# Optimization experiments

Hardware: AMD Instinct MI355X
Metric: run time of the kernel (lower is better)

Reference implementation:

```python
import jax, jax.numpy as jnp
import numpy as np

B, N, D = 1, 128, 64
H, DH = 8, 64            # heads, per-head dim; dim_inner = dim*dim_head = 512
DI = H * DH              # 512
L = 2                    # max_degree
S = 1 + 2 * L            # 5 degree slots: (h, r_1..L, x_1..L)
MLP = 1024               # int(2.0 * dim_inner)
EPS = 1e-5


def _ln(x, g):
    m = x.mean(-1, keepdims=True)
    v = ((x - m) ** 2).mean(-1, keepdims=True)
    return (x - m) * jax.lax.rsqrt(v + EPS) * g


def setup_inputs() -> dict:
    key = jax.random.key(0)
    ks = jax.random.split(key, 16)
    rn = lambda k, s, sc=1.0: jax.random.normal(k, s, dtype=jnp.float32) * sc
    return {
        "h": rn(ks[0], (B, N, D)),
        "t_ij": rn(ks[1], (B, N, N, D)),
        "r1": rn(ks[2], (B, N, N, 3)),
        "r2": rn(ks[3], (B, N, N, 5)),
        "x1": rn(ks[4], (B, N, D, 3)),
        "x2": rn(ks[5], (B, N, D, 5)),
        "g_hi": jnp.ones((D,), jnp.float32),
        "g_hj": jnp.ones((D,), jnp.float32),
        "Wq": rn(ks[6], (D, DI), D ** -0.5),
        "Wk": rn(ks[7], (D, DI), D ** -0.5),
        "Wv1": rn(ks[8], (D, MLP), D ** -0.5),
        "bv1": jnp.zeros((MLP,), jnp.float32),
        "Wv2": rn(ks[9], (MLP, S * DI), MLP ** -0.5),
        "bv2": jnp.zeros((S * DI,), jnp.float32),
        "Wp1": rn(ks[10], (D, MLP), D ** -0.5),
        "bp1": jnp.zeros((MLP,), jnp.float32),
        "Wp2": rn(ks[11], (MLP, S * DI), MLP ** -0.5),
        "bp2": jnp.zeros((S * DI,), jnp.float32),
        "Wev": rn(ks[12], (D, S * DI), D ** -0.5),
        "Wc": rn(ks[13], (DI, D), DI ** -0.5),
    }


def reference(h, t_ij, r1, r2, x1, x2, g_hi, g_hj, Wq, Wk, Wv1, bv1, Wv2, bv2,
              Wp1, bp1, Wp2, bp2, Wev, Wc):
    b, n, d = h.shape
    hi, hj = _ln(h, g_hi), _ln(h, g_hj)
    q = (hi @ Wq).reshape(b, n, H, DH).transpose(0, 2, 1, 3)                # b h i d
    k = (hj @ Wk).reshape(b, n, H, DH).transpose(0, 2, 1, 3)                # b h j d
    vals = (jax.nn.silu(hj @ Wv1 + bv1) @ Wv2 + bv2)
    vals = vals.reshape(b, n, S, H, DH).transpose(0, 3, 1, 2, 4)            # b h j s d
    pav = (jax.nn.silu(hj @ Wp1 + bp1) @ Wp2 + bp2)
    pav = pav.reshape(b, n, S, H, DH).transpose(0, 3, 1, 2, 4)              # b h j s d
    # NOTE: source uses to_edge_values for BOTH edge keys and edge values (to_edge_keys is dead code)
    ev = (t_ij @ Wev).reshape(b, n, n, S, H, DH).transpose(0, 4, 1, 2, 3, 5)  # b h i j s d
    sim_num = jnp.einsum('bhid,bhjd->bhij', q, k)                           # b h i j
    sim_den = jnp.einsum('bhid,bhijsd->bhis', q, ev)                        # b h i s
    attn = sim_num[..., None] / sim_den[:, :, :, None, :]                   # b h i j s (quotient attention)
    sea = attn[..., None] * vals[:, :, None] + ev * pav[:, :, None]         # b h i j s d
    out = sea.transpose(0, 2, 3, 4, 1, 5).reshape(b, n, n, S, DI) @ Wc      # b i j s D
    # split sizes (1, L, L) along the s axis: h scale, r_ij scales, x scales
    h_new = h + out[:, :, :, 0, :].sum(axis=2)                              # sum over neighbors j
    xs, rs = (x1, x2), (r1, r2)
    x_new = [jnp.einsum('bjdm,bijd->bidm', xs[l], out[:, :, :, 1 + L + l, :])
             + jnp.einsum('bijm,bijd->bidm', rs[l], out[:, :, :, 1 + l, :])
             for l in range(L)]
    return (h_new, x_new[0], x_new[1])
```

## Files before the change

kernel.cpp:

```cpp
#include <hip/hip_runtime.h>
#include <hip/hip_bf16.h>

typedef __hip_bfloat16 bf16;
typedef __attribute__((ext_vector_type(8))) short short8;
typedef __attribute__((ext_vector_type(4))) float f32x4;

#define NN 128
#define DD_ 64
#define HH_ 8
#define DH_ 64
#define DI_ 512
#define SS_ 5
#define MLPD 1024
#define SDI 2560

__device__ __forceinline__ float wave_sum64(float v) {
#pragma unroll
    for (int off = 32; off > 0; off >>= 1) v += __shfl_xor(v, off, 64);
    return v;
}

__device__ __forceinline__ unsigned short f2bf_u(float f) {
    unsigned u = __float_as_uint(f);
    u += 0x7FFF + ((u >> 16) & 1);
    return (unsigned short)(u >> 16);
}
__device__ __forceinline__ float bfu2f(unsigned short s) {
    return __uint_as_float(((unsigned)s) << 16);
}
__device__ __forceinline__ unsigned pk2(unsigned short a, unsigned short b) {
    return (unsigned)a | ((unsigned)b << 16);
}

__global__ __launch_bounds__(256) void k_front(
    const float* __restrict__ h, const float* __restrict__ ghi, const float* __restrict__ ghj,
    const float* __restrict__ Wq, const float* __restrict__ Wk,
    const float* __restrict__ Wv1, const float* __restrict__ bv1,
    const float* __restrict__ Wp1, const float* __restrict__ bp1,
    float* __restrict__ q, float* __restrict__ k,
    float* __restrict__ a1, float* __restrict__ p1) {
    int i = blockIdx.x, ch = blockIdx.y, t = threadIdx.x;
    int d = t & 63;
    __shared__ float hib[DD_], hjb[DD_];
    float x = h[i * DD_ + d];
    float s = wave_sum64(x);
    float s2 = wave_sum64(x * x);
    float m = s * (1.0f / DD_);
    float v = s2 * (1.0f / DD_) - m * m;
    float r = rsqrtf(v + 1e-5f);
    float xc = (x - m) * r;
    if (t < 64) { hib[d] = xc * ghi[d]; hjb[d] = xc * ghj[d]; }
    __syncthreads();
    {
        int c = ch * 128 + (t & 127);
        const float* W = (t < 128) ? Wq : Wk;
        const float* hb = (t < 128) ? hib : hjb;
        float a = 0.f;
#pragma unroll 8
        for (int dd = 0; dd < DD_; dd++) a += hb[dd] * W[dd * DI_ + c];
        float* dstqk = (t < 128) ? q : k;
        dstqk[i * DI_ + c] = a;
    }
    {
        int c = ch * 256 + t;
        float av = 0.f, ap = 0.f;
#pragma unroll 4
        for (int dd = 0; dd < DD_; dd++) {
            float hv = hjb[dd];
            av += hv * Wv1[dd * MLPD + c];
            ap += hv * Wp1[dd * MLPD + c];
        }
        float xv = av + bv1[c], xp = ap + bp1[c];
        a1[i * MLPD + c] = xv / (1.0f + expf(-xv));
        p1[i * MLPD + c] = xp / (1.0f + expf(-xp));
    }
}

#define KS2 4
__global__ __launch_bounds__(256) void k_mlp2(const float* __restrict__ a1,
                                              const float* __restrict__ p1,
                                              const float* __restrict__ Wv2,
                                              const float* __restrict__ Wp2,
                                              float* __restrict__ part) {
    int ct = blockIdx.x, ks = blockIdx.y, t = threadIdx.x;
    int c0 = ct * 64;
    bool isp = c0 >= 2560;
    int c0l = c0 - (isp ? 2560 : 0);
    const float* __restrict__ src = isp ? p1 : a1;
    const float* __restrict__ W = isp ? Wp2 : Wv2;
    int kbase = ks * 256;
    __shared__ unsigned short Ahi[128][40], Alo[128][40];
    __shared__ unsigned short Bhi[64][40], Blo[64][40];
    int lane = t & 63, wv = t >> 6;
    int l15 = lane & 15, quad = lane >> 4;
    f32x4 acc[2][4];
#pragma unroll
    for (int mt = 0; mt < 2; mt++)
#pragma unroll
        for (int nt = 0; nt < 4; nt++) acc[mt][nt] = (f32x4){0.f, 0.f, 0.f, 0.f};
    int aj = t >> 1, ak = (t & 1) * 16;
    int bc = t & 63, bk = (t >> 6) * 8;
    for (int kc = 0; kc < 8; kc++) {
        int k0 = kbase + kc * 32;
        __syncthreads();
        {
            unsigned short h16[16], l16[16];
            const float* ap = &src[(size_t)aj * MLPD + k0 + ak];
#pragma unroll
            for (int e = 0; e < 16; e += 4) {
                float4 v = *(const float4*)(ap + e);
                float vv[4] = {v.x, v.y, v.z, v.w};
#pragma unroll
                for (int z = 0; z < 4; z++) {
                    unsigned short hb = f2bf_u(vv[z]);
                    h16[e + z] = hb;
                    l16[e + z] = f2bf_u(vv[z] - bfu2f(hb));
                }
            }
            *(uint4*)&Ahi[aj][ak] = make_uint4(pk2(h16[0], h16[1]), pk2(h16[2], h16[3]),
                                               pk2(h16[4], h16[5]), pk2(h16[6], h16[7]));
            *(uint4*)&Ahi[aj][ak + 8] = make_uint4(pk2(h16[8], h16[9]), pk2(h16[10], h16[11]),
                                                   pk2(h16[12], h16[13]), pk2(h16[14], h16[15]));
            *(uint4*)&Alo[aj][ak] = make_uint4(pk2(l16[0], l16[1]), pk2(l16[2], l16[3]),
                                               pk2(l16[4], l16[5]), pk2(l16[6], l16[7]));
            *(uint4*)&Alo[aj][ak + 8] = make_uint4(pk2(l16[8], l16[9]), pk2(l16[10], l16[11]),
                                                   pk2(l16[12], l16[13]), pk2(l16[14], l16[15]));
        }
        {
            unsigned short h8[8], l8[8];
#pragma unroll
            for (int e = 0; e < 8; e++) {
                float v = W[(size_t)(k0 + bk + e) * SDI + c0l + bc];
                unsigned short hb = f2bf_u(v);
                h8[e] = hb;
                l8[e] = f2bf_u(v - bfu2f(hb));
            }
            *(uint4*)&Bhi[bc][bk] = make_uint4(pk2(h8[0], h8[1]), pk2(h8[2], h8[3]),
                                               pk2(h8[4], h8[5]), pk2(h8[6], h8[7]));
            *(uint4*)&Blo[bc][bk] = make_uint4(pk2(l8[0], l8[1]), pk2(l8[2], l8[3]),
                                               pk2(l8[4], l8[5]), pk2(l8[6], l8[7]));
        }
        __syncthreads();
        int ko = quad * 8;
        short8 a_h0 = *(const short8*)&Ahi[(wv * 2 + 0) * 16 + l15][ko];
        short8 a_l0 = *(const short8*)&Alo[(wv * 2 + 0) * 16 + l15][ko];
        short8 a_h1 = *(const short8*)&Ahi[(wv * 2 + 1) * 16 + l15][ko];
        short8 a_l1 = *(const short8*)&Alo[(wv * 2 + 1) * 16 + l15][ko];
#pragma unroll
        for (int nt = 0; nt < 4; nt++) {
            short8 b_h = *(const short8*)&Bhi[nt * 16 + l15][ko];
            short8 b_l = *(const short8*)&Blo[nt * 16 + l15][ko];
            acc[0][nt] = __builtin_amdgcn_mfma_f32_16x16x32_bf16(a_h0, b_h, acc[0][nt], 0, 0, 0);
            acc[0][nt] = __builtin_amdgcn_mfma_f32_16x16x32_bf16(a_h0, b_l, acc[0][nt], 0, 0, 0);
            acc[0][nt] = __builtin_amdgcn_mfma_f32_16x16x32_bf16(a_l0, b_h, acc[0][nt], 0, 0, 0);
            acc[1][nt] = __builtin_amdgcn_mfma_f32_16x16x32_bf16(a_h1, b_h, acc[1][nt], 0, 0, 0);
            acc[1][nt] = __builtin_amdgcn_mfma_f32_16x16x32_bf16(a_h1, b_l, acc[1][nt], 0, 0, 0);
            acc[1][nt] = __builtin_amdgcn_mfma_f32_16x16x32_bf16(a_l1, b_h, acc[1][nt], 0, 0, 0);
        }
    }
#pragma unroll
    for (int mt = 0; mt < 2; mt++)
#pragma unroll
        for (int nt = 0; nt < 4; nt++)
#pragma unroll
            for (int r = 0; r < 4; r++) {
                int j = (wv * 2 + mt) * 16 + quad * 4 + r;
                int cc = c0 + nt * 16 + l15;
                part[(size_t)ks * 655360 + (size_t)j * 5120 + cc] = acc[mt][nt][r];
            }
}

__global__ __launch_bounds__(512) void k_post(const float* __restrict__ part,
                                              const float* __restrict__ bv2,
                                              const float* __restrict__ bp2,
                                              const float* __restrict__ Wc,
                                              float* __restrict__ pav,
                                              float* __restrict__ VC) {
    int j = blockIdx.x, y = blockIdx.y, t = threadIdx.x;
    if (y < 5) {
        int s = y;
        __shared__ float vlds[512];
        int e = s * 512 + t;
        float sum = 0.f;
#pragma unroll
        for (int p = 0; p < KS2; p++) sum += part[(size_t)p * 655360 + (size_t)j * 5120 + e];
        vlds[t] = sum + bv2[e];
        __syncthreads();
        int dd = t & 63;
        int hbase = t - dd;
        float acc = 0.f;
#pragma unroll 8
        for (int d2 = 0; d2 < DH_; d2++) acc += vlds[hbase + d2] * Wc[(size_t)(hbase + d2) * DD_ + dd];
        VC[(size_t)(j * SS_ + s) * DI_ + t] = acc;
    } else {
        int s = y - 5;
        int e = 2560 + s * 512 + t;
        float sum = 0.f;
#pragma unroll
        for (int p = 0; p < KS2; p++) sum += part[(size_t)p * 655360 + (size_t)j * 5120 + e];
        pav[(size_t)j * SDI + s * 512 + t] = sum + bp2[s * 512 + t];
    }
}

__global__ __launch_bounds__(640) void k_den(const float* __restrict__ tij,
                                             const float* __restrict__ Wev,
                                             const float* __restrict__ q,
                                             float* __restrict__ rsd) {
    int i = blockIdx.x, half = blockIdx.y, t = threadIdx.x;
    __shared__ float red[10][64];
    __shared__ float Tl[64];
    __shared__ float ql[DI_];
    int c = t & 63, jw = t >> 6;
    float s = 0.f;
    for (int j = jw; j < NN; j += 10) s += tij[(size_t)(i * NN + j) * DD_ + c];
    red[jw][c] = s;
    if (t < DI_) ql[t] = q[i * DI_ + t];
    __syncthreads();
    if (t < 64) {
        float a = 0.f;
#pragma unroll
        for (int r2 = 0; r2 < 10; r2++) a += red[r2][t];
        Tl[t] = a;
    }
    __syncthreads();
#pragma unroll
    for (int kx = 0; kx < 2; kx++) {
        int u = half * 1280 + kx * 640 + t;
        float ev = 0.f;
#pragma unroll 8
        for (int cc = 0; cc < DD_; cc++) ev += Tl[cc] * Wev[(size_t)cc * SDI + u];
        float den = wave_sum64(ev * ql[u & 511]);
        if ((t & 63) == 0) {
            int g = u >> 6;
            int ss = g >> 3, hh = g & 7;
            rsd[i * 40 + hh * SS_ + ss] = 1.0f / den;
        }
    }
}

__global__ __launch_bounds__(512) void k_simnum(const float* __restrict__ q,
                                                const float* __restrict__ k,
                                                float* __restrict__ sn) {
    int i = blockIdx.x, yh = blockIdx.y, t = threadIdx.x;
    int hh = yh * 4 + (t >> 7), j = t & 127;
    __shared__ float qb[256];
    if (t < 256) qb[t] = q[i * DI_ + yh * 256 + t];
    __syncthreads();
    float a = 0.f;
    const float* kr = &k[(size_t)j * DI_ + hh * DH_];
    const float* qr = &qb[(hh - yh * 4) * DH_];
#pragma unroll 8
    for (int d = 0; d < DH_; d++) a += qr[d] * kr[d];
    sn[i * 1024 + hh * NN + j] = a;
}

#define KCM 64
__global__ __launch_bounds__(256) void k_M(const float* __restrict__ pav,
                                           const float* __restrict__ Wev,
                                           const float* __restrict__ Wc,
                                           float* __restrict__ M) {
    int j = blockIdx.x, s = blockIdx.y, t = threadIdx.x;
    int lane = t & 63, w = t >> 6;
    __shared__ float P[DI_];
    __shared__ unsigned short Ahi[64][72], Alo[64][72];
    __shared__ unsigned short Bhi[64][72], Blo[64][72];
    P[t] = pav[j * SDI + s * DI_ + t];
    P[t + 256] = pav[j * SDI + s * DI_ + t + 256];
    f32x4 acc[4];
#pragma unroll
    for (int n = 0; n < 4; n++) acc[n] = (f32x4){0.f, 0.f, 0.f, 0.f};
    __syncthreads();
    for (int u0 = 0; u0 < DI_; u0 += KCM) {
        {
            int c = t >> 2, ug = (t & 3) * 16;
            const float* wevp = &Wev[(size_t)c * SDI + s * DI_ + u0 + ug];
            unsigned short ah[16], al[16];
#pragma unroll
            for (int e = 0; e < 16; e += 4) {
                float4 wv = *(const float4*)(wevp + e);
                float4 pv = *(const float4*)&P[u0 + ug + e];
                float av[4] = {wv.x * pv.x, wv.y * pv.y, wv.z * pv.z, wv.w * pv.w};
#pragma unroll
                for (int z = 0; z < 4; z++) {
                    unsigned short hh2 = f2bf_u(av[z]);
                    ah[e + z] = hh2;
                    al[e + z] = f2bf_u(av[z] - bfu2f(hh2));
                }
            }
            *(uint4*)&Ahi[c][ug] = make_uint4(pk2(ah[0], ah[1]), pk2(ah[2], ah[3]),
                                              pk2(ah[4], ah[5]), pk2(ah[6], ah[7]));
            *(uint4*)&Ahi[c][ug + 8] = make_uint4(pk2(ah[8], ah[9]), pk2(ah[10], ah[11]),
                                                  pk2(ah[12], ah[13]), pk2(ah[14], ah[15]));
            *(uint4*)&Alo[c][ug] = make_uint4(pk2(al[0], al[1]), pk2(al[2], al[3]),
                                              pk2(al[4], al[5]), pk2(al[6], al[7]));
            *(uint4*)&Alo[c][ug + 8] = make_uint4(pk2(al[8], al[9]), pk2(al[10], al[11]),
                                                  pk2(al[12], al[13]), pk2(al[14], al[15]));
        }
        {
            int dd = t & 63, ub = (t >> 6) * 16;
            unsigned short bh[16], bl[16];
#pragma unroll
            for (int e = 0; e < 16; e++) {
                float v = Wc[(size_t)(u0 + ub + e) * DD_ + dd];
                unsigned short hh2 = f2bf_u(v);
                bh[e] = hh2;
                bl[e] = f2bf_u(v - bfu2f(hh2));
            }
            *(uint4*)&Bhi[dd][ub] = make_uint4(pk2(bh[0], bh[1]), pk2(bh[2], bh[3]),
                                               pk2(bh[4], bh[5]), pk2(bh[6], bh[7]));
            *(uint4*)&Bhi[dd][ub + 8] = make_uint4(pk2(bh[8], bh[9]), pk2(bh[10], bh[11]),
                                                   pk2(bh[12], bh[13]), pk2(bh[14], bh[15]));
            *(uint4*)&Blo[dd][ub] = make_uint4(pk2(bl[0], bl[1]), pk2(bl[2], bl[3]),
                                               pk2(bl[4], bl[5]), pk2(bl[6], bl[7]));
            *(uint4*)&Blo[dd][ub + 8] = make_uint4(pk2(bl[8], bl[9]), pk2(bl[10], bl[11]),
                                                   pk2(bl[12], bl[13]), pk2(bl[14], bl[15]));
        }
        __syncthreads();
#pragma unroll
        for (int kk = 0; kk < 2; kk++) {
            int ko = kk * 32 + (lane >> 4) * 8;
            short8 a_h = *(const short8*)&Ahi[w * 16 + (lane & 15)][ko];
            short8 a_l = *(const short8*)&Alo[w * 16 + (lane & 15)][ko];
#pragma unroll
            for (int n = 0; n < 4; n++) {
                short8 b_h = *(const short8*)&Bhi[n * 16 + (lane & 15)][ko];
                short8 b_l = *(const short8*)&Blo[n * 16 + (lane & 15)][ko];
                acc[n] = __builtin_amdgcn_mfma_f32_16x16x32_bf16(a_h, b_h, acc[n], 0, 0, 0);
                acc[n] = __builtin_amdgcn_mfma_f32_16x16x32_bf16(a_h, b_l, acc[n], 0, 0, 0);
                acc[n] = __builtin_amdgcn_mfma_f32_16x16x32_bf16(a_l, b_h, acc[n], 0, 0, 0);
            }
        }
        __syncthreads();
    }
    float* Mp = &M[(size_t)(j * SS_ + s) * 4096];
#pragma unroll
    for (int n = 0; n < 4; n++)
#pragma unroll
        for (int r = 0; r < 4; r++) {
            int c = w * 16 + (lane >> 4) * 4 + r;
            int dd = n * 16 + (lane & 15);
            Mp[c * 64 + dd] = acc[n][r];
        }
}

__global__ __launch_bounds__(256) void k_out(const float* __restrict__ M, const float* __restrict__ VC,
                                             const float* __restrict__ sn, const float* __restrict__ rsd,
                                             const float* __restrict__ tij, float* __restrict__ outb) {
    int j = blockIdx.x, s = blockIdx.y, t = threadIdx.x;
    int lane = t & 63, wv = t >> 6, l15 = lane & 15, quad = lane >> 4;
    __shared__ unsigned short Ahi[128][40], Alo[128][40];
    __shared__ unsigned short Bhi[64][40], Blo[64][40];
    f32x4 acc[2][4];
#pragma unroll
    for (int mt = 0; mt < 2; mt++)
#pragma unroll
        for (int nt = 0; nt < 4; nt++) acc[mt][nt] = (f32x4){0.f, 0.f, 0.f, 0.f};
    {
        int i = t >> 1, hg = (t & 1) * 4;
        unsigned short h4[4], l4[4];
#pragma unroll
        for (int e = 0; e < 4; e++) {
            int hh_ = hg + e;
            float v = sn[i * 1024 + hh_ * NN + j] * rsd[i * 40 + hh_ * SS_ + s];
            unsigned short hb = f2bf_u(v);
            h4[e] = hb;
            l4[e] = f2bf_u(v - bfu2f(hb));
        }
        *(uint2*)&Ahi[i][hg] = make_uint2(pk2(h4[0], h4[1]), pk2(h4[2], h4[3]));
        *(uint2*)&Alo[i][hg] = make_uint2(pk2(l4[0], l4[1]), pk2(l4[2], l4[3]));
#pragma unroll
        for (int r = 0; r < 2; r++) {
            int idx = t + r * 256;
            if (idx < 384) {
                int ii = idx / 3, g = idx % 3;
                *(uint4*)&Ahi[ii][8 + g * 8] = make_uint4(0, 0, 0, 0);
                *(uint4*)&Alo[ii][8 + g * 8] = make_uint4(0, 0, 0, 0);
            }
        }
        if (t < 64) {
            unsigned short h8[8], l8[8];
#pragma unroll
            for (int e = 0; e < 8; e++) {
                float v = VC[(size_t)(j * SS_ + s) * DI_ + e * 64 + t];
                unsigned short hb = f2bf_u(v);
                h8[e] = hb;
                l8[e] = f2bf_u(v - bfu2f(hb));
            }
            *(uint4*)&Bhi[t][0] = make_uint4(pk2(h8[0], h8[1]), pk2(h8[2], h8[3]),
                                             pk2(h8[4], h8[5]), pk2(h8[6], h8[7]));
            *(uint4*)&Blo[t][0] = make_uint4(pk2(l8[0], l8[1]), pk2(l8[2], l8[3]),
                                             pk2(l8[4], l8[5]), pk2(l8[6], l8[7]));
        } else {
            int idx = t - 64;
            int dd2 = idx / 3, g = idx % 3;
            *(uint4*)&Bhi[dd2][8 + g * 8] = make_uint4(0, 0, 0, 0);
            *(uint4*)&Blo[dd2][8 + g * 8] = make_uint4(0, 0, 0, 0);
        }
    }
    __syncthreads();
    {
        int ko = quad * 8;
        short8 a_h0 = *(const short8*)&Ahi[(wv * 2 + 0) * 16 + l15][ko];
        short8 a_l0 = *(const short8*)&Alo[(wv * 2 + 0) * 16 + l15][ko];
        short8 a_h1 = *(const short8*)&Ahi[(wv * 2 + 1) * 16 + l15][ko];
        short8 a_l1 = *(const short8*)&Alo[(wv * 2 + 1) * 16 + l15][ko];
#pragma unroll
        for (int nt = 0; nt < 4; nt++) {
            short8 b_h = *(const short8*)&Bhi[nt * 16 + l15][ko];
            short8 b_l = *(const short8*)&Blo[nt * 16 + l15][ko];
            acc[0][nt] = __builtin_amdgcn_mfma_f32_16x16x32_bf16(a_h0, b_h, acc[0][nt], 0, 0, 0);
            acc[0][nt] = __builtin_amdgcn_mfma_f32_16x16x32_bf16(a_h0, b_l, acc[0][nt], 0, 0, 0);
            acc[0][nt] = __builtin_amdgcn_mfma_f32_16x16x32_bf16(a_l0, b_h, acc[0][nt], 0, 0, 0);
            acc[1][nt] = __builtin_amdgcn_mfma_f32_16x16x32_bf16(a_h1, b_h, acc[1][nt], 0, 0, 0);
            acc[1][nt] = __builtin_amdgcn_mfma_f32_16x16x32_bf16(a_h1, b_l, acc[1][nt], 0, 0, 0);
            acc[1][nt] = __builtin_amdgcn_mfma_f32_16x16x32_bf16(a_l1, b_h, acc[1][nt], 0, 0, 0);
        }
    }
    for (int kc = 0; kc < 2; kc++) {
        __syncthreads();
        {
            int i = t >> 1, chalf = (t & 1) * 16;
            unsigned short h16[16], l16[16];
            const float* tp = &tij[(size_t)(i * NN + j) * DD_ + kc * 32 + chalf];
#pragma unroll
            for (int e = 0; e < 16; e += 4) {
                float4 v = *(const float4*)(tp + e);
                float vv[4] = {v.x, v.y, v.z, v.w};
#pragma unroll
                for (int z = 0; z < 4; z++) {
                    unsigned short hb = f2bf_u(vv[z]);
                    h16[e + z] = hb;
                    l16[e + z] = f2bf_u(vv[z] - bfu2f(hb));
                }
            }
            *(uint4*)&Ahi[i][chalf] = make_uint4(pk2(h16[0], h16[1]), pk2(h16[2], h16[3]),
                                                 pk2(h16[4], h16[5]), pk2(h16[6], h16[7]));
            *(uint4*)&Ahi[i][chalf + 8] = make_uint4(pk2(h16[8], h16[9]), pk2(h16[10], h16[11]),
                                                     pk2(h16[12], h16[13]), pk2(h16[14], h16[15]));
            *(uint4*)&Alo[i][chalf] = make_uint4(pk2(l16[0], l16[1]), pk2(l16[2], l16[3]),
                                                 pk2(l16[4], l16[5]), pk2(l16[6], l16[7]));
            *(uint4*)&Alo[i][chalf + 8] = make_uint4(pk2(l16[8], l16[9]), pk2(l16[10], l16[11]),
                                                     pk2(l16[12], l16[13]), pk2(l16[14], l16[15]));
        }
        {
            int dd2 = t & 63, cg = (t >> 6) * 8;
            unsigned short h8[8], l8[8];
#pragma unroll
            for (int e = 0; e < 8; e++) {
                float v = M[(size_t)(j * SS_ + s) * 4096 + (size_t)(kc * 32 + cg + e) * 64 + dd2];
                unsigned short hb = f2bf_u(v);
                h8[e] = hb;
                l8[e] = f2bf_u(v - bfu2f(hb));
            }
            *(uint4*)&Bhi[dd2][cg] = make_uint4(pk2(h8[0], h8[1]), pk2(h8[2], h8[3]),
                                                pk2(h8[4], h8[5]), pk2(h8[6], h8[7]));
            *(uint4*)&Blo[dd2][cg] = make_uint4(pk2(l8[0], l8[1]), pk2(l8[2], l8[3]),
                                                pk2(l8[4], l8[5]), pk2(l8[6], l8[7]));
        }
        __syncthreads();
        int ko = quad * 8;
        short8 a_h0 = *(const short8*)&Ahi[(wv * 2 + 0) * 16 + l15][ko];
        short8 a_l0 = *(const short8*)&Alo[(wv * 2 + 0) * 16 + l15][ko];
        short8 a_h1 = *(const short8*)&Ahi[(wv * 2 + 1) * 16 + l15][ko];
        short8 a_l1 = *(const short8*)&Alo[(wv * 2 + 1) * 16 + l15][ko];
#pragma unroll
        for (int nt = 0; nt < 4; nt++) {
            short8 b_h = *(const short8*)&Bhi[nt * 16 + l15][ko];
            short8 b_l = *(const short8*)&Blo[nt * 16 + l15][ko];
            acc[0][nt] = __builtin_amdgcn_mfma_f32_16x16x32_bf16(a_h0, b_h, acc[0][nt], 0, 0, 0);
            acc[0][nt] = __builtin_amdgcn_mfma_f32_16x16x32_bf16(a_h0, b_l, acc[0][nt], 0, 0, 0);
            acc[0][nt] = __builtin_amdgcn_mfma_f32_16x16x32_bf16(a_l0, b_h, acc[0][nt], 0, 0, 0);
            acc[1][nt] = __builtin_amdgcn_mfma_f32_16x16x32_bf16(a_h1, b_h, acc[1][nt], 0, 0, 0);
            acc[1][nt] = __builtin_amdgcn_mfma_f32_16x16x32_bf16(a_h1, b_l, acc[1][nt], 0, 0, 0);
            acc[1][nt] = __builtin_amdgcn_mfma_f32_16x16x32_bf16(a_l1, b_h, acc[1][nt], 0, 0, 0);
        }
    }
#pragma unroll
    for (int mt = 0; mt < 2; mt++)
#pragma unroll
        for (int nt = 0; nt < 4; nt++)
#pragma unroll
            for (int r = 0; r < 4; r++) {
                int i = (wv * 2 + mt) * 16 + quad * 4 + r;
                int dd = nt * 16 + l15;
                outb[((size_t)(i * NN + j) * SS_ + s) * 64 + dd] = acc[mt][nt][r];
            }
}

#define JC 16
#define JPC 8
__global__ void k_red1(const float* __restrict__ outb,
                       const float* __restrict__ r1, const float* __restrict__ r2,
                       const float* __restrict__ x1, const float* __restrict__ x2,
                       float* __restrict__ pr) {
    int i = blockIdx.x, jc = blockIdx.y, t = threadIdx.x;
    int s = t >> 6, dd = t & 63;
    int jbeg = jc * JPC;
    float hacc = 0.f;
    float am[5] = {0.f, 0.f, 0.f, 0.f, 0.f};
    for (int jj = 0; jj < JPC; jj++) {
        int j = jbeg + jj;
        float ov = outb[((size_t)(i * NN + j) * SS_ + s) * 64 + dd];
        if (s == 0) {
            hacc += ov;
        } else if (s == 1) {
#pragma unroll
            for (int m = 0; m < 3; m++) am[m] += r1[(i * NN + j) * 3 + m] * ov;
        } else if (s == 2) {
#pragma unroll
            for (int m = 0; m < 5; m++) am[m] += r2[(i * NN + j) * 5 + m] * ov;
        } else if (s == 3) {
#pragma unroll
            for (int m = 0; m < 3; m++) am[m] += x1[(j * DD_ + dd) * 3 + m] * ov;
        } else {
#pragma unroll
            for (int m = 0; m < 5; m++) am[m] += x2[(j * DD_ + dd) * 5 + m] * ov;
        }
    }
    float* rec = &pr[(size_t)(i * JC + jc) * 1088];
    if (s == 0) {
        rec[dd] = hacc;
    } else if (s == 1) {
#pragma unroll
        for (int m = 0; m < 3; m++) rec[64 + dd * 3 + m] = am[m];
    } else if (s == 2) {
#pragma unroll
        for (int m = 0; m < 5; m++) rec[256 + dd * 5 + m] = am[m];
    } else if (s == 3) {
#pragma unroll
        for (int m = 0; m < 3; m++) rec[576 + dd * 3 + m] = am[m];
    } else {
#pragma unroll
        for (int m = 0; m < 5; m++) rec[768 + dd * 5 + m] = am[m];
    }
}

__global__ void k_red2(const float* __restrict__ pr, const float* __restrict__ h,
                       float* __restrict__ dst) {
    int i = blockIdx.x, t = threadIdx.x;
    int s = t >> 6, dd = t & 63;
    const float* base = &pr[(size_t)i * JC * 1088];
    if (s == 0) {
        float v = 0.f;
#pragma unroll
        for (int c = 0; c < JC; c++) v += base[c * 1088 + dd];
        dst[i * DD_ + dd] = h[i * DD_ + dd] + v;
    } else if (s == 3) {
        float v[3] = {0.f, 0.f, 0.f};
#pragma unroll
        for (int c = 0; c < JC; c++) {
#pragma unroll
            for (int m = 0; m < 3; m++)
                v[m] += base[c * 1088 + 64 + dd * 3 + m] + base[c * 1088 + 576 + dd * 3 + m];
        }
#pragma unroll
        for (int m = 0; m < 3; m++)
            dst[8192 + (i * DD_ + dd) * 3 + m] = v[m];
    } else if (s == 4) {
        float v[5] = {0.f, 0.f, 0.f, 0.f, 0.f};
#pragma unroll
        for (int c = 0; c < JC; c++) {
#pragma unroll
            for (int m = 0; m < 5; m++)
                v[m] += base[c * 1088 + 256 + dd * 5 + m] + base[c * 1088 + 768 + dd * 5 + m];
        }
#pragma unroll
        for (int m = 0; m < 5; m++)
            dst[8192 + 24576 + (i * DD_ + dd) * 5 + m] = v[m];
    }
}

extern "C" void kernel_launch(void* const* d_in, const int* in_sizes, int n_in,
                              void* d_out, int out_size, void* d_ws, size_t ws_size,
                              hipStream_t stream) {
    const float* h_in = (const float*)d_in[0];
    const float* tij = (const float*)d_in[1];
    const float* r1 = (const float*)d_in[2];
    const float* r2 = (const float*)d_in[3];
    const float* x1 = (const float*)d_in[4];
    const float* x2 = (const float*)d_in[5];
    const float* ghi = (const float*)d_in[6];
    const float* ghj = (const float*)d_in[7];
    const float* Wq = (const float*)d_in[8];
    const float* Wk = (const float*)d_in[9];
    const float* Wv1 = (const float*)d_in[10];
    const float* bv1 = (const float*)d_in[11];
    const float* Wv2 = (const float*)d_in[12];
    const float* bv2 = (const float*)d_in[13];
    const float* Wp1 = (const float*)d_in[14];
    const float* bp1 = (const float*)d_in[15];
    const float* Wp2 = (const float*)d_in[16];
    const float* bp2 = (const float*)d_in[17];
    const float* Wev = (const float*)d_in[18];
    const float* Wc = (const float*)d_in[19];
    float* dst = (float*)d_out;

    float* w = (float*)d_ws;
    size_t off = 16;
    auto alloc = [&](size_t n) { float* p = w + off; off += n; return p; };
    float* q    = alloc(65536);
    float* k    = alloc(65536);
    float* a1   = alloc(131072);
    float* p1   = alloc(131072);
    float* pav  = alloc(327680);
    float* VC   = alloc(327680);
    float* sn   = alloc(131072);
    float* rsd  = alloc(5120);
    float* M    = alloc(2621440);
    float* outb = alloc(5242880);
    float* part = alloc(2621440);
    float* pr   = alloc(2228224);

    k_front<<<dim3(128, 4), dim3(256), 0, stream>>>(h_in, ghi, ghj, Wq, Wk, Wv1, bv1, Wp1, bp1,
                                                    q, k, a1, p1);
    k_mlp2<<<dim3(80, KS2), dim3(256), 0, stream>>>(a1, p1, Wv2, Wp2, part);
    k_post<<<dim3(128, 10), dim3(512), 0, stream>>>(part, bv2, bp2, Wc, pav, VC);
    k_den<<<dim3(128, 2), dim3(640), 0, stream>>>(tij, Wev, q, rsd);
    k_simnum<<<dim3(128, 2), dim3(512), 0, stream>>>(q, k, sn);
    k_M<<<dim3(128, 5), dim3(256), 0, stream>>>(pav, Wev, Wc, M);
    k_out<<<dim3(128, 5), dim3(256), 0, stream>>>(M, VC, sn, rsd, tij, outb);
    k_red1<<<dim3(128, JC), dim3(320), 0, stream>>>(outb, r1, r2, x1, x2, pr);
    k_red2<<<dim3(128), dim3(320), 0, stream>>>(pr, h_in, dst);
}
```

Baseline: 203.9 us.

## Fuse post/M, den/simnum, and out/red1 kernels to cut launches and buffers

```diff
diff --git a/kernel.cpp b/kernel.cpp
--- a/kernel.cpp
+++ b/kernel.cpp
@@ -13,6 +13,13 @@
 #define SS_ 5
 #define MLPD 1024
 #define SDI 2560
+
+#define PR_B0 0
+#define PR_B1 262144
+#define PR_B2 1048576
+#define PR_B3 2359296
+#define PR_B4 3145728
+#define PR_TOT 4456448
 
 __device__ __forceinline__ float wave_sum64(float v) {
 #pragma unroll
@@ -170,116 +177,58 @@
             }
 }
 
-__global__ __launch_bounds__(512) void k_post(const float* __restrict__ part,
-                                              const float* __restrict__ bv2,
-                                              const float* __restrict__ bp2,
-                                              const float* __restrict__ Wc,
-                                              float* __restrict__ pav,
-                                              float* __restrict__ VC) {
-    int j = blockIdx.x, y = blockIdx.y, t = threadIdx.x;
-    if (y < 5) {
-        int s = y;
-        __shared__ float vlds[512];
-        int e = s * 512 + t;
-        float sum = 0.f;
-#pragma unroll
-        for (int p = 0; p < KS2; p++) sum += part[(size_t)p * 655360 + (size_t)j * 5120 + e];
-        vlds[t] = sum + bv2[e];
-        __syncthreads();
-        int dd = t & 63;
-        int hbase = t - dd;
-        float acc = 0.f;
-#pragma unroll 8
-        for (int d2 = 0; d2 < DH_; d2++) acc += vlds[hbase + d2] * Wc[(size_t)(hbase + d2) * DD_ + dd];
-        VC[(size_t)(j * SS_ + s) * DI_ + t] = acc;
-    } else {
-        int s = y - 5;
-        int e = 2560 + s * 512 + t;
-        float sum = 0.f;
-#pragma unroll
-        for (int p = 0; p < KS2; p++) sum += part[(size_t)p * 655360 + (size_t)j * 5120 + e];
-        pav[(size_t)j * SDI + s * 512 + t] = sum + bp2[s * 512 + t];
-    }
-}
-
-__global__ __launch_bounds__(640) void k_den(const float* __restrict__ tij,
-                                             const float* __restrict__ Wev,
-                                             const float* __restrict__ q,
-                                             float* __restrict__ rsd) {
-    int i = blockIdx.x, half = blockIdx.y, t = threadIdx.x;
-    __shared__ float red[10][64];
-    __shared__ float Tl[64];
-    __shared__ float ql[DI_];
-    int c = t & 63, jw = t >> 6;
-    float s = 0.f;
-    for (int j = jw; j < NN; j += 10) s += tij[(size_t)(i * NN + j) * DD_ + c];
-    red[jw][c] = s;
-    if (t < DI_) ql[t] = q[i * DI_ + t];
-    __syncthreads();
-    if (t < 64) {
-        float a = 0.f;
-#pragma unroll
-        for (int r2 = 0; r2 < 10; r2++) a += red[r2][t];
-        Tl[t] = a;
-    }
-    __syncthreads();
-#pragma unroll
-    for (int kx = 0; kx < 2; kx++) {
-        int u = half * 1280 + kx * 640 + t;
-        float ev = 0.f;
-#pragma unroll 8
-        for (int cc = 0; cc < DD_; cc++) ev += Tl[cc] * Wev[(size_t)cc * SDI + u];
-        float den = wave_sum64(ev * ql[u & 511]);
-        if ((t & 63) == 0) {
-            int g = u >> 6;
-            int ss = g >> 3, hh = g & 7;
-            rsd[i * 40 + hh * SS_ + ss] = 1.0f / den;
-        }
-    }
-}
-
-__global__ __launch_bounds__(512) void k_simnum(const float* __restrict__ q,
-                                                const float* __restrict__ k,
-                                                float* __restrict__ sn) {
-    int i = blockIdx.x, yh = blockIdx.y, t = threadIdx.x;
-    int hh = yh * 4 + (t >> 7), j = t & 127;
-    __shared__ float qb[256];
-    if (t < 256) qb[t] = q[i * DI_ + yh * 256 + t];
-    __syncthreads();
-    float a = 0.f;
-    const float* kr = &k[(size_t)j * DI_ + hh * DH_];
-    const float* qr = &qb[(hh - yh * 4) * DH_];
-#pragma unroll 8
-    for (int d = 0; d < DH_; d++) a += qr[d] * kr[d];
-    sn[i * 1024 + hh * NN + j] = a;
-}
-
-#define KCM 64
-__global__ __launch_bounds__(256) void k_M(const float* __restrict__ pav,
-                                           const float* __restrict__ Wev,
-                                           const float* __restrict__ Wc,
-                                           float* __restrict__ M) {
+__global__ __launch_bounds__(256) void k_postM(const float* __restrict__ part,
+                                               const float* __restrict__ bv2,
+                                               const float* __restrict__ bp2,
+                                               const float* __restrict__ Wc,
+                                               const float* __restrict__ Wev,
+                                               float* __restrict__ VC,
+                                               float* __restrict__ M) {
     int j = blockIdx.x, s = blockIdx.y, t = threadIdx.x;
     int lane = t & 63, w = t >> 6;
+    __shared__ float vlds[DI_];
     __shared__ float P[DI_];
     __shared__ unsigned short Ahi[64][72], Alo[64][72];
     __shared__ unsigned short Bhi[64][72], Blo[64][72];
-    P[t] = pav[j * SDI + s * DI_ + t];
-    P[t + 256] = pav[j * SDI + s * DI_ + t + 256];
+#pragma unroll
+    for (int r = 0; r < 2; r++) {
+        int o = t + r * 256;
+        int ev = s * 512 + o;
+        int ep = 2560 + s * 512 + o;
+        float sv = 0.f, sp = 0.f;
+#pragma unroll
+        for (int p = 0; p < KS2; p++) {
+            sv += part[(size_t)p * 655360 + (size_t)j * 5120 + ev];
+            sp += part[(size_t)p * 655360 + (size_t)j * 5120 + ep];
+        }
+        vlds[o] = sv + bv2[ev];
+        P[o] = sp + bp2[s * 512 + o];
+    }
+    __syncthreads();
+#pragma unroll
+    for (int r = 0; r < 2; r++) {
+        int o = t + r * 256;
+        int dd = o & 63;
+        int hb = o - dd;
+        float acc2 = 0.f;
+#pragma unroll 8
+        for (int d2 = 0; d2 < DH_; d2++) acc2 += vlds[hb + d2] * Wc[(size_t)(hb + d2) * DD_ + dd];
+        VC[(size_t)(j * SS_ + s) * DI_ + o] = acc2;
+    }
     f32x4 acc[4];
 #pragma unroll
     for (int n = 0; n < 4; n++) acc[n] = (f32x4){0.f, 0.f, 0.f, 0.f};
-    __syncthreads();
-    for (int u0 = 0; u0 < DI_; u0 += KCM) {
+    for (int u0 = 0; u0 < DI_; u0 += 64) {
+        __syncthreads();
         {
             int c = t >> 2, ug = (t & 3) * 16;
             const float* wevp = &Wev[(size_t)c * SDI + s * DI_ + u0 + ug];
             unsigned short ah[16], al[16];
 #pragma unroll
             for (int e = 0; e < 16; e += 4) {
-                float4 wv = *(const float4*)(wevp + e);
+                float4 wv2 = *(const float4*)(wevp + e);
                 float4 pv = *(const float4*)&P[u0 + ug + e];
-                float av[4] = {wv.x * pv.x, wv.y * pv.y, wv.z * pv.z, wv.w * pv.w};
+                float av[4] = {wv2.x * pv.x, wv2.y * pv.y, wv2.z * pv.z, wv2.w * pv.w};
 #pragma unroll
                 for (int z = 0; z < 4; z++) {
                     unsigned short hh2 = f2bf_u(av[z]);
@@ -330,7 +279,6 @@
                 acc[n] = __builtin_amdgcn_mfma_f32_16x16x32_bf16(a_l, b_h, acc[n], 0, 0, 0);
             }
         }
-        __syncthreads();
     }
     float* Mp = &M[(size_t)(j * SS_ + s) * 4096];
 #pragma unroll
@@ -343,195 +291,235 @@
         }
 }
 
-__global__ __launch_bounds__(256) void k_out(const float* __restrict__ M, const float* __restrict__ VC,
-                                             const float* __restrict__ sn, const float* __restrict__ rsd,
-                                             const float* __restrict__ tij, float* __restrict__ outb) {
-    int j = blockIdx.x, s = blockIdx.y, t = threadIdx.x;
+__global__ __launch_bounds__(640) void k_densim(const float* __restrict__ tij,
+                                                const float* __restrict__ Wev,
+                                                const float* __restrict__ q,
+                                                const float* __restrict__ k,
+                                                float* __restrict__ rsd,
+                                                float* __restrict__ sn) {
+    int i = blockIdx.x, y = blockIdx.y, t = threadIdx.x;
+    __shared__ float red[10][64];
+    __shared__ float Tl[64];
+    __shared__ float ql[DI_];
+    if (y < 2) {
+        int half = y;
+        int c = t & 63, jw = t >> 6;
+        float s = 0.f;
+        for (int j = jw; j < NN; j += 10) s += tij[(size_t)(i * NN + j) * DD_ + c];
+        red[jw][c] = s;
+        if (t < DI_) ql[t] = q[i * DI_ + t];
+        __syncthreads();
+        if (t < 64) {
+            float a = 0.f;
+#pragma unroll
+            for (int r2 = 0; r2 < 10; r2++) a += red[r2][t];
+            Tl[t] = a;
+        }
+        __syncthreads();
+#pragma unroll
+        for (int kx = 0; kx < 2; kx++) {
+            int u = half * 1280 + kx * 640 + t;
+            float ev = 0.f;
+#pragma unroll 8
+            for (int cc = 0; cc < DD_; cc++) ev += Tl[cc] * Wev[(size_t)cc * SDI + u];
+            float den = wave_sum64(ev * ql[u & 511]);
+            if ((t & 63) == 0) {
+                int g = u >> 6;
+                int ss = g >> 3, hh = g & 7;
+                rsd[i * 40 + hh * SS_ + ss] = 1.0f / den;
+            }
+        }
+    } else {
+        if (t < DI_) ql[t] = q[i * DI_ + t];
+        __syncthreads();
+        for (int e = t; e < 1024; e += 640) {
+            int hh = e >> 7, j = e & 127;
+            float a = 0.f;
+            const float* kr = &k[(size_t)j * DI_ + hh * DH_];
+            const float* qr = &ql[hh * DH_];
+#pragma unroll 8
+            for (int d = 0; d < DH_; d++) a += qr[d] * kr[d];
+            sn[i * 1024 + hh * NN + j] = a;
+        }
+    }
+}
+
+__global__ __launch_bounds__(256) void k_outred(
+    const float* __restrict__ M, const float* __restrict__ VC,
+    const float* __restrict__ sn, const float* __restrict__ rsd,
+    const float* __restrict__ tij,
+    const float* __restrict__ r1, const float* __restrict__ r2,
+    const float* __restrict__ x1, const float* __restrict__ x2,
+    float* __restrict__ pr) {
+    int jc = blockIdx.x, s = blockIdx.y, ic = blockIdx.z, t = threadIdx.x;
     int lane = t & 63, wv = t >> 6, l15 = lane & 15, quad = lane >> 4;
-    __shared__ unsigned short Ahi[128][40], Alo[128][40];
+    __shared__ unsigned short Ahi[64][40], Alo[64][40];
     __shared__ unsigned short Bhi[64][40], Blo[64][40];
-    f32x4 acc[2][4];
-#pragma unroll
-    for (int mt = 0; mt < 2; mt++)
-#pragma unroll
-        for (int nt = 0; nt < 4; nt++) acc[mt][nt] = (f32x4){0.f, 0.f, 0.f, 0.f};
-    {
-        int i = t >> 1, hg = (t & 1) * 4;
-        unsigned short h4[4], l4[4];
-#pragma unroll
-        for (int e = 0; e < 4; e++) {
-            int hh_ = hg + e;
-            float v = sn[i * 1024 + hh_ * NN + j] * rsd[i * 40 + hh_ * SS_ + s];
-            unsigned short hb = f2bf_u(v);
-            h4[e] = hb;
-            l4[e] = f2bf_u(v - bfu2f(hb));
-        }
-        *(uint2*)&Ahi[i][hg] = make_uint2(pk2(h4[0], h4[1]), pk2(h4[2], h4[3]));
-        *(uint2*)&Alo[i][hg] = make_uint2(pk2(l4[0], l4[1]), pk2(l4[2], l4[3]));
-#pragma unroll
-        for (int r = 0; r < 2; r++) {
-            int idx = t + r * 256;
-            if (idx < 384) {
-                int ii = idx / 3, g = idx % 3;
-                *(uint4*)&Ahi[ii][8 + g * 8] = make_uint4(0, 0, 0, 0);
-                *(uint4*)&Alo[ii][8 + g * 8] = make_uint4(0, 0, 0, 0);
-            }
-        }
-        if (t < 64) {
-            unsigned short h8[8], l8[8];
-#pragma unroll
-            for (int e = 0; e < 8; e++) {
-                float v = VC[(size_t)(j * SS_ + s) * DI_ + e * 64 + t];
-                unsigned short hb = f2bf_u(v);
-                h8[e] = hb;
-                l8[e] = f2bf_u(v - bfu2f(hb));
-            }
-            *(uint4*)&Bhi[t][0] = make_uint4(pk2(h8[0], h8[1]), pk2(h8[2], h8[3]),
-                                             pk2(h8[4], h8[5]), pk2(h8[6], h8[7]));
-            *(uint4*)&Blo[t][0] = make_uint4(pk2(l8[0], l8[1]), pk2(l8[2], l8[3]),
-                                             pk2(l8[4], l8[5]), pk2(l8[6], l8[7]));
+    __shared__ float wl[320];
+    int Lm = (s == 2 || s == 4) ? 5 : 3;
+    float accW[5][4][4];
+#pragma unroll
+    for (int m = 0; m < 5; m++)
+#pragma unroll
+        for (int nt = 0; nt < 4; nt++)
+#pragma unroll
+            for (int r = 0; r < 4; r++) accW[m][nt][r] = 0.f;
+    int i0 = ic * 64;
+    for (int jj = 0; jj < 4; jj++) {
+        int j = jc * 4 + jj;
+        f32x4 acc_o[4];
+#pragma unroll
+        for (int nt = 0; nt < 4; nt++) acc_o[nt] = (f32x4){0.f, 0.f, 0.f, 0.f};
+        __syncthreads();
+        if (s == 1) {
+            for (int e = t; e < 192; e += 256) wl[e] = r1[((i0 + e / 3) * NN + j) * 3 + e % 3];
+        } else if (s == 2) {
+            for (int e = t; e < 320; e += 256) wl[e] = r2[((i0 + e / 5) * NN + j) * 5 + e % 5];
+        } else if (s == 3) {
+            for (int e = t; e < 192; e += 256) wl[e] = x1[((size_t)j * DD_ + e / 3) * 3 + e % 3];
+        } else if (s == 4) {
+            for (int e = t; e < 320; e += 256) wl[e] = x2[((size_t)j * DD_ + e / 5) * 5 + e % 5];
+        }
+        {
+            int il = t >> 2, hg = (t & 3) * 2;
+            int ii = i0 + il;
+            float v0 = sn[ii * 1024 + hg * NN + j] * rsd[ii * 40 + hg * SS_ + s];
+            float v1 = sn[ii * 1024 + (hg + 1) * NN + j] * rsd[ii * 40 + (hg + 1) * SS_ + s];
+            unsigned short h0 = f2bf_u(v0), h1 = f2bf_u(v1);
+            unsigned short g0 = f2bf_u(v0 - bfu2f(h0)), g1 = f2bf_u(v1 - bfu2f(h1));
+            *(unsigned*)&Ahi[il][hg] = pk2(h0, h1);
+            *(unsigned*)&Alo[il][hg] = pk2(g0, g1);
+            if (t < 192) {
+                int row = t / 3, g = t % 3;
+                *(uint4*)&Ahi[row][8 + g * 8] = make_uint4(0, 0, 0, 0);
+                *(uint4*)&Alo[row][8 + g * 8] = make_uint4(0, 0, 0, 0);
+            }
+            if (t < 64) {
+                unsigned short h8[8], l8[8];
+#pragma unroll
+                for (int e = 0; e < 8; e++) {
+                    float v = VC[(size_t)(j * SS_ + s) * DI_ + e * 64 + t];
+                    unsigned short hb = f2bf_u(v);
+                    h8[e] = hb;
+                    l8[e] = f2bf_u(v - bfu2f(hb));
+                }
+                *(uint4*)&Bhi[t][0] = make_uint4(pk2(h8[0], h8[1]), pk2(h8[2], h8[3]),
+                                                 pk2(h8[4], h8[5]), pk2(h8[6], h8[7]));
+                *(uint4*)&Blo[t][0] = make_uint4(pk2(l8[0], l8[1]), pk2(l8[2], l8[3]),
+                                                 pk2(l8[4], l8[5]), pk2(l8[6], l8[7]));
+            } else {
+                int idx = t - 64;
+                int row = idx / 3, g = idx % 3;
+                *(uint4*)&Bhi[row][8 + g * 8] = make_uint4(0, 0, 0, 0);
+                *(uint4*)&Blo[row][8 + g * 8] = make_uint4(0, 0, 0, 0);
+            }
+        }
+        __syncthreads();
+        {
+            int ko = quad * 8;
+            short8 a_h = *(const short8*)&Ahi[wv * 16 + l15][ko];
+            short8 a_l = *(const short8*)&Alo[wv * 16 + l15][ko];
+#pragma unroll
+            for (int nt = 0; nt < 4; nt++) {
+                short8 b_h = *(const short8*)&Bhi[nt * 16 + l15][ko];
+                short8 b_l = *(const short8*)&Blo[nt * 16 + l15][ko];
+                acc_o[nt] = __builtin_amdgcn_mfma_f32_16x16x32_bf16(a_h, b_h, acc_o[nt], 0, 0, 0);
+                acc_o[nt] = __builtin_amdgcn_mfma_f32_16x16x32_bf16(a_h, b_l, acc_o[nt], 0, 0, 0);
+                acc_o[nt] = __builtin_amdgcn_mfma_f32_16x16x32_bf16(a_l, b_h, acc_o[nt], 0, 0, 0);
+            }
+        }
+        for (int kc = 0; kc < 2; kc++) {
+            __syncthreads();
+            {
+                int il = t >> 2, cg = (t & 3) * 8;
+                const float* tp = &tij[(size_t)((i0 + il) * NN + j) * DD_ + kc * 32 + cg];
+                float4 va = *(const float4*)tp;
+                float4 vb = *(const float4*)(tp + 4);
+                float vv[8] = {va.x, va.y, va.z, va.w, vb.x, vb.y, vb.z, vb.w};
+                unsigned short h8[8], l8[8];
+#pragma unroll
+                for (int z = 0; z < 8; z++) {
+                    unsigned short hb = f2bf_u(vv[z]);
+                    h8[z] = hb;
+                    l8[z] = f2bf_u(vv[z] - bfu2f(hb));
+                }
+                *(uint4*)&Ahi[il][cg] = make_uint4(pk2(h8[0], h8[1]), pk2(h8[2], h8[3]),
+                                                   pk2(h8[4], h8[5]), pk2(h8[6], h8[7]));
+                *(uint4*)&Alo[il][cg] = make_uint4(pk2(l8[0], l8[1]), pk2(l8[2], l8[3]),
+                                                   pk2(l8[4], l8[5]), pk2(l8[6], l8[7]));
+            }
+            {
+                int dd = t & 63, cg = (t >> 6) * 8;
+                unsigned short h8[8], l8[8];
+#pragma unroll
+                for (int e = 0; e < 8; e++) {
+                    float v = M[(size_t)(j * SS_ + s) * 4096 + (size_t)(kc * 32 + cg + e) * 64 + dd];
+                    unsigned short hb = f2bf_u(v);
+                    h8[e] = hb;
+                    l8[e] = f2bf_u(v - bfu2f(hb));
+                }
+                *(uint4*)&Bhi[dd][cg] = make_uint4(pk2(h8[0], h8[1]), pk2(h8[2], h8[3]),
+                                                   pk2(h8[4], h8[5]), pk2(h8[6], h8[7]));
+                *(uint4*)&Blo[dd][cg] = make_uint4(pk2(l8[0], l8[1]), pk2(l8[2], l8[3]),
+                                                   pk2(l8[4], l8[5]), pk2(l8[6], l8[7]));
+            }
+            __syncthreads();
+            int ko = quad * 8;
+            short8 a_h = *(const short8*)&Ahi[wv * 16 + l15][ko];
+            short8 a_l = *(const short8*)&Alo[wv * 16 + l15][ko];
+#pragma unroll
+            for (int nt = 0; nt < 4; nt++) {
+                short8 b_h = *(const short8*)&Bhi[nt * 16 + l15][ko];
+                short8 b_l = *(const short8*)&Blo[nt * 16 + l15][ko];
+                acc_o[nt] = __builtin_amdgcn_mfma_f32_16x16x32_bf16(a_h, b_h, acc_o[nt], 0, 0, 0);
+                acc_o[nt] = __builtin_amdgcn_mfma_f32_16x16x32_bf16(a_h, b_l, acc_o[nt], 0, 0, 0);
+                acc_o[nt] = __builtin_amdgcn_mfma_f32_16x16x32_bf16(a_l, b_h, acc_o[nt], 0, 0, 0);
+            }
+        }
+        if (s == 0) {
+#pragma unroll
+            for (int nt = 0; nt < 4; nt++)
+#pragma unroll
+                for (int r = 0; r < 4; r++) accW[0][nt][r] += acc_o[nt][r];
+        } else if (s <= 2) {
+            int rb = wv * 16 + quad * 4;
+            for (int m = 0; m < Lm; m++)
+#pragma unroll
+                for (int r = 0; r < 4; r++) {
+                    float wgt = wl[(rb + r) * Lm + m];
+#pragma unroll
+                    for (int nt = 0; nt < 4; nt++) accW[m][nt][r] += wgt * acc_o[nt][r];
+                }
         } else {
-            int idx = t - 64;
-            int dd2 = idx / 3, g = idx % 3;
-            *(uint4*)&Bhi[dd2][8 + g * 8] = make_uint4(0, 0, 0, 0);
-            *(uint4*)&Blo[dd2][8 + g * 8] = make_uint4(0, 0, 0, 0);
-        }
-    }
-    __syncthreads();
-    {
-        int ko = quad * 8;
-        short8 a_h0 = *(const short8*)&Ahi[(wv * 2 + 0) * 16 + l15][ko];
-        short8 a_l0 = *(const short8*)&Alo[(wv * 2 + 0) * 16 + l15][ko];
-        short8 a_h1 = *(const short8*)&Ahi[(wv * 2 + 1) * 16 + l15][ko];
-        short8 a_l1 = *(const short8*)&Alo[(wv * 2 + 1) * 16 + l15][ko];
-#pragma unroll
-        for (int nt = 0; nt < 4; nt++) {
-            short8 b_h = *(const short8*)&Bhi[nt * 16 + l15][ko];
-            short8 b_l = *(const short8*)&Blo[nt * 16 + l15][ko];
-            acc[0][nt] = __builtin_amdgcn_mfma_f32_16x16x32_bf16(a_h0, b_h, acc[0][nt], 0, 0, 0);
-            acc[0][nt] = __builtin_amdgcn_mfma_f32_16x16x32_bf16(a_h0, b_l, acc[0][nt], 0, 0, 0);
-            acc[0][nt] = __builtin_amdgcn_mfma_f32_16x16x32_bf16(a_l0, b_h, acc[0][nt], 0, 0, 0);
-            acc[1][nt] = __builtin_amdgcn_mfma_f32_16x16x32_bf16(a_h1, b_h, acc[1][nt], 0, 0, 0);
-            acc[1][nt] = __builtin_amdgcn_mfma_f32_16x16x32_bf16(a_h1, b_l, acc[1][nt], 0, 0, 0);
-            acc[1][nt] = __builtin_amdgcn_mfma_f32_16x16x32_bf16(a_l1, b_h, acc[1][nt], 0, 0, 0);
-        }
-    }
-    for (int kc = 0; kc < 2; kc++) {
-        __syncthreads();
-        {
-            int i = t >> 1, chalf = (t & 1) * 16;
-            unsigned short h16[16], l16[16];
-            const float* tp = &tij[(size_t)(i * NN + j) * DD_ + kc * 32 + chalf];
-#pragma unroll
-            for (int e = 0; e < 16; e += 4) {
-                float4 v = *(const float4*)(tp + e);
-                float vv[4] = {v.x, v.y, v.z, v.w};
-#pragma unroll
-                for (int z = 0; z < 4; z++) {
-                    unsigned short hb = f2bf_u(vv[z]);
-                    h16[e + z] = hb;
-                    l16[e + z] = f2bf_u(vv[z] - bfu2f(hb));
-                }
-            }
-            *(uint4*)&Ahi[i][chalf] = make_uint4(pk2(h16[0], h16[1]), pk2(h16[2], h16[3]),
-                                                 pk2(h16[4], h16[5]), pk2(h16[6], h16[7]));
-            *(uint4*)&Ahi[i][chalf + 8] = make_uint4(pk2(h16[8], h16[9]), pk2(h16[10], h16[11]),
-                                                     pk2(h16[12], h16[13]), pk2(h16[14], h16[15]));
-            *(uint4*)&Alo[i][chalf] = make_uint4(pk2(l16[0], l16[1]), pk2(l16[2], l16[3]),
-                                                 pk2(l16[4], l16[5]), pk2(l16[6], l16[7]));
-            *(uint4*)&Alo[i][chalf + 8] = make_uint4(pk2(l16[8], l16[9]), pk2(l16[10], l16[11]),
-                                                     pk2(l16[12], l16[13]), pk2(l16[14], l16[15]));
-        }
-        {
-            int dd2 = t & 63, cg = (t >> 6) * 8;
-            unsigned short h8[8], l8[8];
-#pragma unroll
-            for (int e = 0; e < 8; e++) {
-                float v = M[(size_t)(j * SS_ + s) * 4096 + (size_t)(kc * 32 + cg + e) * 64 + dd2];
-                unsigned short hb = f2bf_u(v);
-                h8[e] = hb;
-                l8[e] = f2bf_u(v - bfu2f(hb));
-            }
-            *(uint4*)&Bhi[dd2][cg] = make_uint4(pk2(h8[0], h8[1]), pk2(h8[2], h8[3]),
-                                                pk2(h8[4], h8[5]), pk2(h8[6], h8[7]));
-            *(uint4*)&Blo[dd2][cg] = make_uint4(pk2(l8[0], l8[1]), pk2(l8[2], l8[3]),
-                                                pk2(l8[4], l8[5]), pk2(l8[6], l8[7]));
-        }
-        __syncthreads();
-        int ko = quad * 8;
-        short8 a_h0 = *(const short8*)&Ahi[(wv * 2 + 0) * 16 + l15][ko];
-        short8 a_l0 = *(const short8*)&Alo[(wv * 2 + 0) * 16 + l15][ko];
-        short8 a_h1 = *(const short8*)&Ahi[(wv * 2 + 1) * 16 + l15][ko];
-        short8 a_l1 = *(const short8*)&Alo[(wv * 2 + 1) * 16 + l15][ko];
-#pragma unroll
-        for (int nt = 0; nt < 4; nt++) {
-            short8 b_h = *(const short8*)&Bhi[nt * 16 + l15][ko];
-            short8 b_l = *(const short8*)&Blo[nt * 16 + l15][ko];
-            acc[0][nt] = __builtin_amdgcn_mfma_f32_16x16x32_bf16(a_h0, b_h, acc[0][nt], 0, 0, 0);
-            acc[0][nt] = __builtin_amdgcn_mfma_f32_16x16x32_bf16(a_h0, b_l, acc[0][nt], 0, 0, 0);
-            acc[0][nt] = __builtin_amdgcn_mfma_f32_16x16x32_bf16(a_l0, b_h, acc[0][nt], 0, 0, 0);
-            acc[1][nt] = __builtin_amdgcn_mfma_f32_16x16x32_bf16(a_h1, b_h, acc[1][nt], 0, 0, 0);
-            acc[1][nt] = __builtin_amdgcn_mfma_f32_16x16x32_bf16(a_h1, b_l, acc[1][nt], 0, 0, 0);
-            acc[1][nt] = __builtin_amdgcn_mfma_f32_16x16x32_bf16(a_l1, b_h, acc[1][nt], 0, 0, 0);
-        }
-    }
-#pragma unroll
-    for (int mt = 0; mt < 2; mt++)
+            for (int m = 0; m < Lm; m++)
+#pragma unroll
+                for (int nt = 0; nt < 4; nt++) {
+                    float wgt = wl[(nt * 16 + l15) * Lm + m];
+#pragma unroll
+                    for (int r = 0; r < 4; r++) accW[m][nt][r] += wgt * acc_o[nt][r];
+                }
+        }
+    }
+    size_t base = (s == 0) ? PR_B0 : (s == 1) ? PR_B1 : (s == 2) ? PR_B2 : (s == 3) ? PR_B3 : PR_B4;
+    if (s == 0) {
 #pragma unroll
         for (int nt = 0; nt < 4; nt++)
 #pragma unroll
             for (int r = 0; r < 4; r++) {
-                int i = (wv * 2 + mt) * 16 + quad * 4 + r;
+                int i = i0 + wv * 16 + quad * 4 + r;
                 int dd = nt * 16 + l15;
-                outb[((size_t)(i * NN + j) * SS_ + s) * 64 + dd] = acc[mt][nt][r];
-            }
-}
-
-#define JC 16
-#define JPC 8
-__global__ void k_red1(const float* __restrict__ outb,
-                       const float* __restrict__ r1, const float* __restrict__ r2,
-                       const float* __restrict__ x1, const float* __restrict__ x2,
-                       float* __restrict__ pr) {
-    int i = blockIdx.x, jc = blockIdx.y, t = threadIdx.x;
-    int s = t >> 6, dd = t & 63;
-    int jbeg = jc * JPC;
-    float hacc = 0.f;
-    float am[5] = {0.f, 0.f, 0.f, 0.f, 0.f};
-    for (int jj = 0; jj < JPC; jj++) {
-        int j = jbeg + jj;
-        float ov = outb[((size_t)(i * NN + j) * SS_ + s) * 64 + dd];
-        if (s == 0) {
-            hacc += ov;
-        } else if (s == 1) {
-#pragma unroll
-            for (int m = 0; m < 3; m++) am[m] += r1[(i * NN + j) * 3 + m] * ov;
-        } else if (s == 2) {
-#pragma unroll
-            for (int m = 0; m < 5; m++) am[m] += r2[(i * NN + j) * 5 + m] * ov;
-        } else if (s == 3) {
-#pragma unroll
-            for (int m = 0; m < 3; m++) am[m] += x1[(j * DD_ + dd) * 3 + m] * ov;
-        } else {
-#pragma unroll
-            for (int m = 0; m < 5; m++) am[m] += x2[(j * DD_ + dd) * 5 + m] * ov;
-        }
-    }
-    float* rec = &pr[(size_t)(i * JC + jc) * 1088];
-    if (s == 0) {
-        rec[dd] = hacc;
-    } else if (s == 1) {
-#pragma unroll
-        for (int m = 0; m < 3; m++) rec[64 + dd * 3 + m] = am[m];
-    } else if (s == 2) {
-#pragma unroll
-        for (int m = 0; m < 5; m++) rec[256 + dd * 5 + m] = am[m];
-    } else if (s == 3) {
-#pragma unroll
-        for (int m = 0; m < 3; m++) rec[576 + dd * 3 + m] = am[m];
+                pr[base + ((size_t)(jc * 128 + i)) * 64 + dd] = accW[0][nt][r];
+            }
     } else {
-#pragma unroll
-        for (int m = 0; m < 5; m++) rec[768 + dd * 5 + m] = am[m];
+        for (int m = 0; m < Lm; m++)
+#pragma unroll
+            for (int nt = 0; nt < 4; nt++)
+#pragma unroll
+                for (int r = 0; r < 4; r++) {
+                    int i = i0 + wv * 16 + quad * 4 + r;
+                    int dd = nt * 16 + l15;
+                    pr[base + (((size_t)(jc * 128 + i)) * 64 + dd) * Lm + m] = accW[m][nt][r];
+                }
     }
 }
 
@@ -539,30 +527,28 @@
                        float* __restrict__ dst) {
     int i = blockIdx.x, t = threadIdx.x;
     int s = t >> 6, dd = t & 63;
-    const float* base = &pr[(size_t)i * JC * 1088];
     if (s == 0) {
         float v = 0.f;
-#pragma unroll
-        for (int c = 0; c < JC; c++) v += base[c * 1088 + dd];
+        for (int c = 0; c < 32; c++) v += pr[PR_B0 + ((size_t)(c * 128 + i)) * 64 + dd];
         dst[i * DD_ + dd] = h[i * DD_ + dd] + v;
     } else if (s == 3) {
         float v[3] = {0.f, 0.f, 0.f};
-#pragma unroll
-        for (int c = 0; c < JC; c++) {
+        for (int c = 0; c < 32; c++) {
+            size_t ro = ((size_t)(c * 128 + i)) * 64 + dd;
 #pragma unroll
             for (int m = 0; m < 3; m++)
-                v[m] += base[c * 1088 + 64 + dd * 3 + m] + base[c * 1088 + 576 + dd * 3 + m];
+                v[m] += pr[PR_B1 + ro * 3 + m] + pr[PR_B3 + ro * 3 + m];
         }
 #pragma unroll
         for (int m = 0; m < 3; m++)
             dst[8192 + (i * DD_ + dd) * 3 + m] = v[m];
     } else if (s == 4) {
         float v[5] = {0.f, 0.f, 0.f, 0.f, 0.f};
-#pragma unroll
-        for (int c = 0; c < JC; c++) {
+        for (int c = 0; c < 32; c++) {
+            size_t ro = ((size_t)(c * 128 + i)) * 64 + dd;
 #pragma unroll
             for (int m = 0; m < 5; m++)
-                v[m] += base[c * 1088 + 256 + dd * 5 + m] + base[c * 1088 + 768 + dd * 5 + m];
+                v[m] += pr[PR_B2 + ro * 5 + m] + pr[PR_B4 + ro * 5 + m];
         }
 #pragma unroll
         for (int m = 0; m < 5; m++)
@@ -602,23 +588,18 @@
     float* k    = alloc(65536);
     float* a1   = alloc(131072);
     float* p1   = alloc(131072);
-    float* pav  = alloc(327680);
     float* VC   = alloc(327680);
     float* sn   = alloc(131072);
     float* rsd  = alloc(5120);
     float* M    = alloc(2621440);
-    float* outb = alloc(5242880);
     float* part = alloc(2621440);
-    float* pr   = alloc(2228224);
+    float* pr   = alloc(PR_TOT);
 
     k_front<<<dim3(128, 4), dim3(256), 0, stream>>>(h_in, ghi, ghj, Wq, Wk, Wv1, bv1, Wp1, bp1,
                                                     q, k, a1, p1);
     k_mlp2<<<dim3(80, KS2), dim3(256), 0, stream>>>(a1, p1, Wv2, Wp2, part);
-    k_post<<<dim3(128, 10), dim3(512), 0, stream>>>(part, bv2, bp2, Wc, pav, VC);
-    k_den<<<dim3(128, 2), dim3(640), 0, stream>>>(tij, Wev, q, rsd);
-    k_simnum<<<dim3(128, 2), dim3(512), 0, stream>>>(q, k, sn);
-    k_M<<<dim3(128, 5), dim3(256), 0, stream>>>(pav, Wev, Wc, M);
-    k_out<<<dim3(128, 5), dim3(256), 0, stream>>>(M, VC, sn, rsd, tij, outb);
-    k_red1<<<dim3(128, JC), dim3(320), 0, stream>>>(outb, r1, r2, x1, x2, pr);
+    k_densim<<<dim3(128, 3), dim3(640), 0, stream>>>(tij, Wev, q, k, rsd, sn);
+    k_postM<<<dim3(128, 5), dim3(256), 0, stream>>>(part, bv2, bp2, Wc, Wev, VC, M);
+    k_outred<<<dim3(32, 5, 2), dim3(256), 0, stream>>>(M, VC, sn, rsd, tij, r1, r2, x1, x2, pr);
     k_red2<<<dim3(128), dim3(320), 0, stream>>>(pr, h_in, dst);
 }
```

Measured after the change: 241.1 us. 18.3% more time.
